# Optimization experiments

Hardware: AMD Instinct MI355X
Metric: run time of the kernel (lower is better)

The kernel has to match this reference:

```python
import jax, jax.numpy as jnp
import numpy as np

B, T, D, H = 2, 2048, 1024, 16
DK = D // H
NEG = -1e9  # stand-in for -inf; causal mask guarantees >=1 valid key per row


def setup_inputs() -> dict:
    key = jax.random.key(0)
    ks = jax.random.split(key, 9)
    s = 1.0 / np.sqrt(D)
    x = jax.random.normal(ks[0], (B, T, D), dtype=jnp.float32)
    mask = jnp.broadcast_to(jnp.tril(jnp.ones((T, T), dtype=jnp.int32))[None, None], (B, 1, T, T))
    params = {}
    for i, n in enumerate(['q', 'k', 'v', 'o']):
        params['W' + n] = jax.random.normal(ks[1 + 2 * i], (D, D), dtype=jnp.float32) * s
        params['b' + n] = jax.random.normal(ks[2 + 2 * i], (D,), dtype=jnp.float32) * s
    return dict(x=x, mask=mask, **params)


def reference(x, mask, Wq, bq, Wk, bk, Wv, bv, Wo, bo):
    Bx, Tx, Dx = x.shape
    # projections: [B,T,D] -> [B,H,T,DK]
    def split_heads(y):
        return y.reshape(Bx, Tx, H, DK).transpose(0, 2, 1, 3)
    Q = split_heads(x @ Wq + bq)
    K = split_heads(x @ Wk + bk)
    V = split_heads(x @ Wv + bv)
    scores = jnp.einsum('bhqd,bhkd->bhqk', Q, K) / jnp.sqrt(jnp.float32(DK))
    scores = jnp.where(mask == 0, NEG, scores)
    attn = jax.nn.softmax(scores, axis=-1)  # dropout is identity in eval / p=0
    out = jnp.einsum('bhqk,bhkd->bhqd', attn, V)
    out = out.transpose(0, 2, 1, 3).reshape(Bx, Tx, Dx)
    return out @ Wo + bo
```

## Files before the change

### kernel.cpp

```cpp
#include <hip/hip_runtime.h>
#include <hip/hip_bf16.h>

typedef __bf16 bf16;
typedef __attribute__((ext_vector_type(8))) __bf16 bf16x8;
typedef __attribute__((ext_vector_type(4))) __bf16 bf16x4;
typedef __attribute__((ext_vector_type(4))) float f32x4;
typedef __attribute__((ext_vector_type(16))) float f32x16;
typedef __attribute__((ext_vector_type(4))) int int4v;

#define TSEQ 2048
#define DMODEL 1024
#define NHEAD 16
#define DKH 64
#define BATCH 2
#define NQKV 3072

typedef __attribute__((address_space(1))) const void gv_t;
typedef __attribute__((address_space(3))) void sv_t;
__device__ __forceinline__ void gll16(const bf16* g, bf16* s) {
    __builtin_amdgcn_global_load_lds((gv_t*)g, (sv_t*)s, 16, 0, 0);
}
#define WAIT_VM(n) __builtin_amdgcn_s_waitcnt(0x0F70 | (n))

__device__ __forceinline__ unsigned cvtpk(float lo, float hi) {
    unsigned d;
    asm("v_cvt_pk_bf16_f32 %0, %1, %2" : "=v"(d) : "v"(lo), "v"(hi));
    return d;
}

#define PREP_CONV 4096
#define PREP_TW   4096
#define PREP_GRID (PREP_CONV + PREP_TW + 12)
__global__ __launch_bounds__(256) void prep(
    const float* __restrict__ x,
    const float* __restrict__ Wq, const float* __restrict__ Wk,
    const float* __restrict__ Wv, const float* __restrict__ Wo,
    const float* __restrict__ bq, const float* __restrict__ bk,
    const float* __restrict__ bv,
    bf16* __restrict__ xb, bf16* __restrict__ WT, float* __restrict__ biasO)
{
    __shared__ float t[32][33];
    int bid = blockIdx.x;
    const int tid = threadIdx.x;
    if (bid < PREP_CONV) {
        int i = (bid * 256 + tid) * 4;
        f32x4 v = *(const f32x4*)(x + i);
        bf16x4 o;
#pragma unroll
        for (int j = 0; j < 4; ++j) o[j] = (bf16)v[j];
        *(bf16x4*)(xb + i) = o;
        return;
    }
    bid -= PREP_CONV;
    if (bid < PREP_TW) {
        int z = bid >> 10;
        int by = ((bid >> 5) & 31) * 32, bx = (bid & 31) * 32;
        const float* W = z == 0 ? Wq : z == 1 ? Wk : z == 2 ? Wv : Wo;
        bf16* T = WT + (size_t)z * DMODEL * DMODEL;
        int tx = tid & 31, ty = tid >> 5;
#pragma unroll
        for (int i = 0; i < 4; ++i)
            t[ty + i * 8][tx] = W[(size_t)(by + ty + i * 8) * DMODEL + bx + tx];
        __syncthreads();
#pragma unroll
        for (int i = 0; i < 4; ++i)
            T[(size_t)(bx + ty + i * 8) * DMODEL + by + tx] = (bf16)t[tx][ty + i * 8];
        return;
    }
    bid -= PREP_TW;
    int i = bid * 256 + tid;
    float v = i < 1024 ? bq[i] : i < 2048 ? bk[i - 1024] : bv[i - 2048];
    biasO[i] = v;
}

template <typename OutT, int NW_N, bool FUSE_VT>
__global__ __launch_bounds__(256) void gemm_bias_kernel(
    const bf16* __restrict__ A, const bf16* __restrict__ BT,
    const float* __restrict__ bias, OutT* __restrict__ C, int ldc,
    bf16* __restrict__ VT)
{
    constexpr int BN    = NW_N * 64;
    constexpr int MW    = 4 / NW_N;
    constexpr int WROWS = 128 / MW;
    constexpr int FM    = WROWS / 16;
    constexpr int ASZ   = 128 * 32;
    constexpr int BSZ   = BN * 32;
    constexpr int BNP   = BN + 4;
    constexpr int TST   = 136;
    constexpr int EPI   = sizeof(OutT) == 2 ? (FUSE_VT ? 128 * TST : 128 * BN)
                                            : 64 * BNP * 2;
    constexpr int STG   = 2 * ASZ + 2 * BSZ;
    constexpr int SMEM  = STG > EPI ? STG : EPI;
    __shared__ bf16 smem[SMEM];
    bf16* As0 = smem;
    bf16* Bs0 = smem + 2 * ASZ;

    const int tid = threadIdx.x;
    const int ln = tid & 63, wave = tid >> 6;
    const int wm = NW_N == 2 ? (wave >> 1) : wave;
    const int wn = NW_N == 2 ? (wave & 1) : 0;
    const int lr = ln & 15, quad = ln >> 4;
    const int m0 = blockIdx.y * 128, n0 = blockIdx.x * BN;

    f32x4 acc[FM][4] = {};

    const int grow = ln >> 2;
    const int gcol = (ln & 3) * 8;
    const bf16* Ag = A + (size_t)(m0 + wave * 32 + grow) * DMODEL + gcol;
    const bf16* Bg = BT + (size_t)(n0 + (NW_N == 2 ? wave * 32 : wave * 16) + grow) * DMODEL + gcol;

    auto stage = [&](int buf, int kk) {
        bf16* AsW = As0 + buf * ASZ + wave * 1024;
        gll16(Ag + kk, AsW);
        gll16(Ag + (size_t)16 * DMODEL + kk, AsW + 512);
        if constexpr (NW_N == 2) {
            bf16* BsW = Bs0 + buf * BSZ + wave * 1024;
            gll16(Bg + kk, BsW);
            gll16(Bg + (size_t)16 * DMODEL + kk, BsW + 512);
        } else {
            gll16(Bg + kk, Bs0 + buf * BSZ + wave * 512);
        }
    };

    constexpr int NT = DMODEL / 32;
    stage(0, 0);
    WAIT_VM(0);
    __syncthreads();
    for (int kt = 0; kt < NT; ++kt) {
        if (kt + 1 < NT) stage((kt + 1) & 1, (kt + 1) * 32);
        const bf16* AsB = As0 + (kt & 1) * ASZ;
        const bf16* BsB = Bs0 + (kt & 1) * BSZ;
        bf16x8 af[FM], bfr[4];
#pragma unroll
        for (int i = 0; i < FM; ++i)
            af[i] = *(const bf16x8*)(AsB + (wm * WROWS + i * 16 + lr) * 32 + quad * 8);
#pragma unroll
        for (int j = 0; j < 4; ++j)
            bfr[j] = *(const bf16x8*)(BsB + (wn * 64 + j * 16 + lr) * 32 + quad * 8);
#pragma unroll
        for (int i = 0; i < FM; ++i)
#pragma unroll
            for (int j = 0; j < 4; ++j)
                acc[i][j] = __builtin_amdgcn_mfma_f32_16x16x32_bf16(
                    af[i], bfr[j], acc[i][j], 0, 0, 0);
        WAIT_VM(0);
        __syncthreads();
    }

    if constexpr (sizeof(OutT) == 2) {
        if (FUSE_VT && n0 >= 2048) {
            bf16* Cs = smem;
#pragma unroll
            for (int j = 0; j < 4; ++j) {
                int nl = wn * 64 + j * 16 + lr;
                float bv = bias[n0 + nl];
#pragma unroll
                for (int i = 0; i < FM; ++i) {
                    int ml = wm * WROWS + i * 16 + quad * 4;
#pragma unroll
                    for (int r = 0; r < 4; ++r)
                        Cs[nl * TST + ml + r] = (bf16)(acc[i][j][r] + bv);
                }
            }
            __syncthreads();
            const int bb = m0 >> 11;
            const int tloc = m0 & 2047;
#pragma unroll
            for (int p = 0; p < 8; ++p) {
                int dl = p * 16 + (tid >> 4);
                int t0 = (tid & 15) * 8;
                bf16x8 v = *(const bf16x8*)(Cs + dl * TST + t0);
                *(bf16x8*)(VT + (size_t)(bb * 1024 + (n0 - 2048) + dl) * TSEQ +
                           tloc + t0) = v;
            }
            return;
        }
        bf16* Cs = smem;
#pragma unroll
        for (int j = 0; j < 4; ++j) {
            int nl = wn * 64 + j * 16 + lr;
            float bv = bias[n0 + nl];
#pragma unroll
            for (int i = 0; i < FM; ++i) {
                int ml = wm * WROWS + i * 16 + quad * 4;
#pragma unroll
                for (int r = 0; r < 4; ++r)
                    Cs[(ml + r) * BN + nl] = (bf16)(acc[i][j][r] + bv);
            }
        }
        __syncthreads();
        constexpr int LPR = BN / 8;
        constexpr int RPP = 256 / LPR;
        const int rr = tid / LPR, cc = (tid % LPR) * 8;
#pragma unroll
        for (int p = 0; p < 128 / RPP; ++p) {
            int row = p * RPP + rr;
            *(bf16x8*)(C + (size_t)(m0 + row) * ldc + n0 + cc) =
                *(const bf16x8*)(Cs + row * BN + cc);
        }
    } else {
        float* Cf = (float*)smem;
#pragma unroll
        for (int half = 0; half < 2; ++half) {
            if (((wm * WROWS) >> 6) == half) {
#pragma unroll
                for (int j = 0; j < 4; ++j) {
                    int nl = wn * 64 + j * 16 + lr;
                    float bv = bias[n0 + nl];
#pragma unroll
                    for (int i = 0; i < FM; ++i) {
                        int ml = wm * WROWS + i * 16 + quad * 4 - half * 64;
#pragma unroll
                        for (int r = 0; r < 4; ++r)
                            Cf[(ml + r) * BNP + nl] = acc[i][j][r] + bv;
                    }
                }
            }
            __syncthreads();
            constexpr int LPR = BN / 4;
            constexpr int RPP = 256 / LPR;
            const int rr = tid / LPR, cc = (tid % LPR) * 4;
#pragma unroll
            for (int p = 0; p < 64 / RPP; ++p) {
                int row = p * RPP + rr;
                *(f32x4*)(C + (size_t)(m0 + half * 64 + row) * ldc + n0 + cc) =
                    *(const f32x4*)(Cf + row * BNP + cc);
            }
            __syncthreads();
        }
    }
}

template <int KTN, bool MASKED>
__device__ __forceinline__ void tile_step(
    int kt0, int kc, int qabs,
    const bf16* __restrict__ Ksb, const bf16* __restrict__ Vsb,
    const bf16x8 qf[4], f32x16 oacc[2], float& lrow,
    int ln31, int hi, int sw)
{
    f32x16 st[KTN] = {};
#pragma unroll
    for (int t = 0; t < KTN; ++t)
#pragma unroll
        for (int ks = 0; ks < 4; ++ks) {
            const bf16x8 ka = *(const bf16x8*)(
                Ksb + (ln31 + (kt0 + t) * 32) * 64 + (((2 * ks + hi) ^ sw) * 8));
            st[t] = __builtin_amdgcn_mfma_f32_32x32x16_bf16(ka, qf[ks], st[t], 0, 0, 0);
        }

    const float scale2 = 0.18033688f;
    float rs = 0.f;
#pragma unroll
    for (int t = 0; t < KTN; ++t)
#pragma unroll
        for (int r = 0; r < 16; ++r) {
            float p = exp2f(fmaf(st[t][r], scale2, -24.0f));
            if (MASKED &&
                (kc + (kt0 + t) * 32 + (r & 3) + 8 * (r >> 2) + 4 * hi > qabs))
                p = 0.f;
            rs += p;
            st[t][r] = p;
        }
    rs += __shfl_xor(rs, 32);
    lrow += rs;

#pragma unroll
    for (int t = 0; t < KTN; ++t)
#pragma unroll
        for (int s2 = 0; s2 < 2; ++s2) {
            const int bb = s2 * 8;
            unsigned c01 = cvtpk(st[t][bb + 0], st[t][bb + 1]);
            unsigned c23 = cvtpk(st[t][bb + 2], st[t][bb + 3]);
            unsigned c45 = cvtpk(st[t][bb + 4], st[t][bb + 5]);
            unsigned c67 = cvtpk(st[t][bb + 6], st[t][bb + 7]);
            asm("v_permlane32_swap_b32 %0, %1" : "+v"(c01), "+v"(c45));
            asm("v_permlane32_swap_b32 %0, %1" : "+v"(c23), "+v"(c67));
            int4v pw;
            pw[0] = (int)c01; pw[1] = (int)c23; pw[2] = (int)c45; pw[3] = (int)c67;
            const bf16x8 pa = __builtin_bit_cast(bf16x8, pw);
            const int ksg = (kt0 + t) * 2 + s2;
#pragma unroll
            for (int dblk = 0; dblk < 2; ++dblk) {
                const bf16x8 vb = *(const bf16x8*)(
                    Vsb + (dblk * 32 + ln31) * 64 + (((2 * ksg + hi) ^ sw) * 8));
                oacc[dblk] = __builtin_amdgcn_mfma_f32_32x32x16_bf16(
                    pa, vb, oacc[dblk], 0, 0, 0);
            }
        }
}

__global__ __launch_bounds__(256, 2) void flash_attn(
    const bf16* __restrict__ QKV, const bf16* __restrict__ VT,
    bf16* __restrict__ O)
{
    __shared__ bf16 Ks[2][64 * 64];
    __shared__ bf16 Vs[2][64 * 64];
    const int tid = threadIdx.x;
    const int ln = tid & 63, w = tid >> 6;
    const int ln31 = ln & 31, hi = ln >> 5, sw = ln & 7;
    const int wg = blockIdx.x;
    const int g = wg & 31, p = wg >> 5;
    const int h = g >> 1, b = g & 1;
    const int q0A = p * 64, q0B = (31 - p) * 64;

    const bf16* Qb = QKV + (size_t)b * TSEQ * NQKV + h * DKH;
    const bf16* Kb = Qb + 1024;
    const bf16* VTb = VT + (size_t)(b * NHEAD + h) * DKH * TSEQ;

    const int q1 = (w < 2 ? q0A : q0B) + (w & 1) * 32 + ln31;
    const int q2 = q0B + (w & 1) * 32 + ln31;

    bf16x8 qf1[4], qf2[4];
#pragma unroll
    for (int ks = 0; ks < 4; ++ks) {
        qf1[ks] = *(const bf16x8*)(Qb + (size_t)q1 * NQKV + ks * 16 + hi * 8);
        qf2[ks] = *(const bf16x8*)(Qb + (size_t)q2 * NQKV + ks * 16 + hi * 8);
    }
    WAIT_VM(0);

    const int srow = (w & 1) * 32 + (ln >> 3);
    const int scol = ((ln & 7) ^ ((ln >> 3) & 7)) * 8;
    const bool stK = (w < 2);
    auto stage = [&](int buf, int kc) {
        if (stK) {
            const bf16* g2 = Kb + (size_t)(kc + srow) * NQKV + scol;
            bf16* s = &Ks[buf][(w & 1) * 32 * 64];
#pragma unroll
            for (int l = 0; l < 4; ++l)
                gll16(g2 + (size_t)(l * 8) * NQKV, s + l * 8 * 64);
        } else {
            const bf16* g2 = VTb + (size_t)srow * TSEQ + kc + scol;
            bf16* s = &Vs[buf][(w & 1) * 32 * 64];
#pragma unroll
            for (int l = 0; l < 4; ++l)
                gll16(g2 + (size_t)(l * 8) * TSEQ, s + l * 8 * 64);
        }
    };

    f32x16 oacc1[2] = {}, oacc2[2] = {};
    float l1 = 0.f, l2 = 0.f;

    const int nld = 32 - p;
    stage(0, 0);
    WAIT_VM(0);
    __syncthreads();
    for (int c = 0; c < nld; ++c) {
        if (c + 1 < nld) stage((c + 1) & 1, (c + 1) * 64);
        const int kc = c * 64;
        const bf16* K = Ks[c & 1];
        const bf16* V = Vs[c & 1];
        if (c <= p) {
            if (w < 2 && c == p)
                tile_step<2, true >(0, kc, q1, K, V, qf1, oacc1, l1, ln31, hi, sw);
            else
                tile_step<2, false>(0, kc, q1, K, V, qf1, oacc1, l1, ln31, hi, sw);
        } else {
            const int kt0 = w >> 1;
            if (c == nld - 1)
                tile_step<1, true >(kt0, kc, q2, K, V, qf2, oacc2, l2, ln31, hi, sw);
            else
                tile_step<1, false>(kt0, kc, q2, K, V, qf2, oacc2, l2, ln31, hi, sw);
        }
        WAIT_VM(0);
        __syncthreads();
    }

    float* exO = (float*)&Ks[0][0];
    float* exL = (float*)&Vs[0][0];
    if (w < 2) {
        float* dst = exO + w * 2048;
#pragma unroll
        for (int dblk = 0; dblk < 2; ++dblk)
#pragma unroll
            for (int r = 0; r < 16; ++r) {
                int q = (r & 3) + 8 * (r >> 2) + 4 * hi;
                dst[q * 64 + dblk * 32 + ln31] = oacc2[dblk][r];
            }
        if (ln < 32) exL[w * 32 + ln] = l2;
    }
    __syncthreads();

    f32x16 oat[2];
    float lt;
    int qs;
    if (w < 2) {
        oat[0] = oacc1[0]; oat[1] = oacc1[1];
        lt = l1;
        qs = q0A + (w & 1) * 32;
    } else {
        const float* src = exO + (w - 2) * 2048;
        lt = l1 + l2 + exL[(w - 2) * 32 + ln31];
#pragma unroll
        for (int dblk = 0; dblk < 2; ++dblk)
#pragma unroll
            for (int r = 0; r < 16; ++r) {
                int q = (r & 3) + 8 * (r >> 2) + 4 * hi;
                oat[dblk][r] = oacc1[dblk][r] + oacc2[dblk][r] +
                               src[q * 64 + dblk * 32 + ln31];
            }
        qs = q0B + (w & 1) * 32;
    }

#pragma unroll
    for (int r = 0; r < 16; ++r) {
        const int crow = (r & 3) + 8 * (r >> 2) + 4 * hi;
        const float inv = 1.0f / __shfl(lt, crow);
        const int row = qs + crow;
#pragma unroll
        for (int dblk = 0; dblk < 2; ++dblk)
            O[(size_t)(b * TSEQ + row) * DMODEL + h * DKH + dblk * 32 + ln31] =
                (bf16)(oat[dblk][r] * inv);
    }
}

extern "C" void kernel_launch(void* const* d_in, const int* in_sizes, int n_in,
                              void* d_out, int out_size, void* d_ws, size_t ws_size,
                              hipStream_t stream)
{
    const float* x  = (const float*)d_in[0];
    const float* Wq = (const float*)d_in[2];
    const float* bq = (const float*)d_in[3];
    const float* Wk = (const float*)d_in[4];
    const float* bk = (const float*)d_in[5];
    const float* Wv = (const float*)d_in[6];
    const float* bv = (const float*)d_in[7];
    const float* Wo = (const float*)d_in[8];
    const float* bo = (const float*)d_in[9];

    char* ws = (char*)d_ws;
    bf16* xb   = (bf16*)(ws);
    bf16* QKV  = (bf16*)(ws + (8u  << 20));
    bf16* VT   = (bf16*)(ws + (32u << 20));
    bf16* O    = (bf16*)(ws + (40u << 20));
    bf16* WT   = (bf16*)(ws + (48u << 20));
    float* wsBias = (float*)O;

    prep<<<PREP_GRID, 256, 0, stream>>>(x, Wq, Wk, Wv, Wo, bq, bk, bv,
                                        xb, WT, wsBias);

    gemm_bias_kernel<bf16, 2, true><<<dim3(NQKV / 128, 32), 256, 0, stream>>>(
        xb, WT, wsBias, QKV, NQKV, VT);

    flash_attn<<<512, 256, 0, stream>>>(QKV, VT, O);

    gemm_bias_kernel<float, 1, false><<<dim3(DMODEL / 64, 32), 256, 0, stream>>>(
        O, WT + 3u * (1u << 20), bo, (float*)d_out, DMODEL, nullptr);
}
```

Before: 209.1 us.

## Deepen GEMM and attention load pipelines and raise MFMA wave priority

The projection GEMM moves from double to triple buffering in LDS, waiting with partial vmcnt so two k-tiles stay in flight and one barrier per iteration is removed. The attention kernel grows to four K/V buffers and handles two chunks per barrier, prefetching two chunks ahead. MFMA sections in tile_step are wrapped with s_setprio to favour matrix issue. Trade-offs are more LDS per block, which may cut occupancy (attention now uses 64KB per block at 2 blocks per CU), and a riskier partial-wait count that must match the exact number of outstanding loads.

```diff
diff --git a/kernel.cpp b/kernel.cpp
--- a/kernel.cpp
+++ b/kernel.cpp
@@ -89,11 +89,11 @@
     constexpr int TST   = 136;
     constexpr int EPI   = sizeof(OutT) == 2 ? (FUSE_VT ? 128 * TST : 128 * BN)
                                             : 64 * BNP * 2;
-    constexpr int STG   = 2 * ASZ + 2 * BSZ;
+    constexpr int STG   = 3 * ASZ + 3 * BSZ;
     constexpr int SMEM  = STG > EPI ? STG : EPI;
     __shared__ bf16 smem[SMEM];
     bf16* As0 = smem;
-    bf16* Bs0 = smem + 2 * ASZ;
+    bf16* Bs0 = smem + 3 * ASZ;
 
     const int tid = threadIdx.x;
     const int ln = tid & 63, wave = tid >> 6;
@@ -124,12 +124,14 @@
 
     constexpr int NT = DMODEL / 32;
     stage(0, 0);
-    WAIT_VM(0);
-    __syncthreads();
-    for (int kt = 0; kt < NT; ++kt) {
-        if (kt + 1 < NT) stage((kt + 1) & 1, (kt + 1) * 32);
-        const bf16* AsB = As0 + (kt & 1) * ASZ;
-        const bf16* BsB = Bs0 + (kt & 1) * BSZ;
+    stage(1, 32);
+    for (int kt = 0, cur = 0; kt < NT; ++kt, cur = cur == 2 ? 0 : cur + 1) {
+        if (kt + 1 < NT) { if constexpr (NW_N == 2) WAIT_VM(4); else WAIT_VM(3); }
+        else WAIT_VM(0);
+        __syncthreads();
+        if (kt + 2 < NT) stage(cur == 0 ? 2 : cur - 1, (kt + 2) * 32);
+        const bf16* AsB = As0 + cur * ASZ;
+        const bf16* BsB = Bs0 + cur * BSZ;
         bf16x8 af[FM], bfr[4];
 #pragma unroll
         for (int i = 0; i < FM; ++i)
@@ -143,9 +145,8 @@
             for (int j = 0; j < 4; ++j)
                 acc[i][j] = __builtin_amdgcn_mfma_f32_16x16x32_bf16(
                     af[i], bfr[j], acc[i][j], 0, 0, 0);
-        WAIT_VM(0);
-        __syncthreads();
-    }
+    }
+    __syncthreads();
 
     if constexpr (sizeof(OutT) == 2) {
         if (FUSE_VT && n0 >= 2048) {
@@ -166,8 +167,8 @@
             const int bb = m0 >> 11;
             const int tloc = m0 & 2047;
 #pragma unroll
-            for (int p = 0; p < 8; ++p) {
-                int dl = p * 16 + (tid >> 4);
+            for (int pp = 0; pp < 8; ++pp) {
+                int dl = pp * 16 + (tid >> 4);
                 int t0 = (tid & 15) * 8;
                 bf16x8 v = *(const bf16x8*)(Cs + dl * TST + t0);
                 *(bf16x8*)(VT + (size_t)(bb * 1024 + (n0 - 2048) + dl) * TSEQ +
@@ -193,8 +194,8 @@
         constexpr int RPP = 256 / LPR;
         const int rr = tid / LPR, cc = (tid % LPR) * 8;
 #pragma unroll
-        for (int p = 0; p < 128 / RPP; ++p) {
-            int row = p * RPP + rr;
+        for (int pp = 0; pp < 128 / RPP; ++pp) {
+            int row = pp * RPP + rr;
             *(bf16x8*)(C + (size_t)(m0 + row) * ldc + n0 + cc) =
                 *(const bf16x8*)(Cs + row * BN + cc);
         }
@@ -221,8 +222,8 @@
             constexpr int RPP = 256 / LPR;
             const int rr = tid / LPR, cc = (tid % LPR) * 4;
 #pragma unroll
-            for (int p = 0; p < 64 / RPP; ++p) {
-                int row = p * RPP + rr;
+            for (int pp = 0; pp < 64 / RPP; ++pp) {
+                int row = pp * RPP + rr;
                 *(f32x4*)(C + (size_t)(m0 + half * 64 + row) * ldc + n0 + cc) =
                     *(const f32x4*)(Cf + row * BNP + cc);
             }
@@ -239,6 +240,7 @@
     int ln31, int hi, int sw)
 {
     f32x16 st[KTN] = {};
+    __builtin_amdgcn_s_setprio(1);
 #pragma unroll
     for (int t = 0; t < KTN; ++t)
 #pragma unroll
@@ -247,6 +249,7 @@
                 Ksb + (ln31 + (kt0 + t) * 32) * 64 + (((2 * ks + hi) ^ sw) * 8));
             st[t] = __builtin_amdgcn_mfma_f32_32x32x16_bf16(ka, qf[ks], st[t], 0, 0, 0);
         }
+    __builtin_amdgcn_s_setprio(0);
 
     const float scale2 = 0.18033688f;
     float rs = 0.f;
@@ -264,6 +267,7 @@
     rs += __shfl_xor(rs, 32);
     lrow += rs;
 
+    __builtin_amdgcn_s_setprio(1);
 #pragma unroll
     for (int t = 0; t < KTN; ++t)
 #pragma unroll
@@ -287,14 +291,15 @@
                     pa, vb, oacc[dblk], 0, 0, 0);
             }
         }
+    __builtin_amdgcn_s_setprio(0);
 }
 
 __global__ __launch_bounds__(256, 2) void flash_attn(
     const bf16* __restrict__ QKV, const bf16* __restrict__ VT,
     bf16* __restrict__ O)
 {
-    __shared__ bf16 Ks[2][64 * 64];
-    __shared__ bf16 Vs[2][64 * 64];
+    __shared__ bf16 Ks[4][64 * 64];
+    __shared__ bf16 Vs[4][64 * 64];
     const int tid = threadIdx.x;
     const int ln = tid & 63, w = tid >> 6;
     const int ln31 = ln & 31, hi = ln >> 5, sw = ln & 7;
@@ -341,14 +346,11 @@
     float l1 = 0.f, l2 = 0.f;
 
     const int nld = 32 - p;
-    stage(0, 0);
-    WAIT_VM(0);
-    __syncthreads();
-    for (int c = 0; c < nld; ++c) {
-        if (c + 1 < nld) stage((c + 1) & 1, (c + 1) * 64);
+
+    auto do_chunk = [&](int c) {
         const int kc = c * 64;
-        const bf16* K = Ks[c & 1];
-        const bf16* V = Vs[c & 1];
+        const bf16* K = Ks[c & 3];
+        const bf16* V = Vs[c & 3];
         if (c <= p) {
             if (w < 2 && c == p)
                 tile_step<2, true >(0, kc, q1, K, V, qf1, oacc1, l1, ln31, hi, sw);
@@ -361,9 +363,19 @@
             else
                 tile_step<1, false>(kt0, kc, q2, K, V, qf2, oacc2, l2, ln31, hi, sw);
         }
+    };
+
+    stage(0, 0);
+    stage(1, 64);
+    for (int c = 0; c < nld; c += 2) {
         WAIT_VM(0);
         __syncthreads();
-    }
+        if (c + 2 < nld) stage((c + 2) & 3, (c + 2) * 64);
+        if (c + 3 < nld) stage((c + 3) & 3, (c + 3) * 64);
+        do_chunk(c);
+        if (c + 1 < nld) do_chunk(c + 1);
+    }
+    __syncthreads();
 
     float* exO = (float*)&Ks[0][0];
     float* exL = (float*)&Vs[0][0];
```

Result: faster. 201.2 us (-3.8%).
